# Kernel optimization log

Hardware: AMD Instinct MI355X
Metric: run time of the kernel (lower is better)

Reference implementation:

```python
import jax, jax.numpy as jnp
import numpy as np

B, S, E, D, H, L, V = 8, 128, 512, 1024, 16, 4, 32000
DH = D // H
FF = 4 * D
SCALE = 1.0 / (DH ** 0.5)
NEG = -1e30


def _layer_norm(x, g, b, eps=1e-5):
    m = jnp.mean(x, axis=-1, keepdims=True)
    v = jnp.mean((x - m) ** 2, axis=-1, keepdims=True)
    return (x - m) / jnp.sqrt(v + eps) * g + b


def _rel_shift(x):
    # x: [q, k, b, n] -> TransformerXL relative shift
    q, k, b, n = x.shape
    xp = jnp.concatenate([jnp.zeros((q, 1, b, n), x.dtype), x], axis=1)
    xp = xp.reshape(k + 1, q, b, n)
    return xp[1:].reshape(q, k, b, n)


def setup_inputs():
    key = jax.random.key(0)
    ks = jax.random.split(key, 40)
    g = lambda i, shape, s=0.02: jax.random.normal(ks[i], shape, jnp.float32) * s
    inp = {
        'input_ids': jax.random.randint(ks[0], (B, E), 0, V),
        'encoder_rep': jax.random.normal(ks[1], (B, E, D), jnp.float32),
        'input_mask': jnp.ones((B, E), jnp.float32),
        'decode_input': jax.random.randint(ks[2], (B, S), 0, V),
        'decode_target': jax.random.randint(ks[3], (B, S), 0, V),
        'word_emb': g(4, (V, D)),
        'qkv_w': g(5, (L, 3 * D, D)), 'r_w': g(6, (L, D, D)), 'o_w': g(7, (L, D, D)),
        'kv_w': g(8, (L, 2 * D, D)), 'q_w': g(9, (L, D, D)), 'io_w': g(10, (L, D, D)),
        'rr_bias': g(11, (L, H, DH)), 'rw_bias': g(12, (L, H, DH)),
        'ln1_g': jnp.ones((L, D)), 'ln1_b': jnp.zeros((L, D)),
        'ln2_g': jnp.ones((L, D)), 'ln2_b': jnp.zeros((L, D)),
        'ffn_w1': g(13, (L, FF, D)), 'ffn_b1': jnp.zeros((L, FF)),
        'ffn_w2': g(14, (L, D, FF)), 'ffn_b2': jnp.zeros((L, D)),
        'ln3_g': jnp.ones((L, D)), 'ln3_b': jnp.zeros((L, D)),
        'out_w': g(15, (D, D)), 'out_b': jnp.zeros((D,)),
        'copy_w': g(16, (D, D)), 'copy_b': jnp.zeros((D,)),
        'mode_w': g(17, (1, D)), 'mode_b': jnp.zeros((1,)),
    }
    return inp


def _forward(input_ids, encoder_rep, input_mask, decode_input, decode_target,
             word_emb, qkv_w, r_w, o_w, kv_w, q_w, io_w, rr_bias, rw_bias,
             ln1_g, ln1_b, ln2_g, ln2_b, ffn_w1, ffn_b1, ffn_w2, ffn_b2,
             ln3_g, ln3_b, out_w, out_b, copy_w, copy_b, mode_w, mode_b):
    # relative position embedding r: [S, D]
    pos_seq = jnp.arange(S - 1, -1, -1.0, dtype=jnp.float32)
    inv_freq = 1.0 / (10000.0 ** (jnp.arange(0.0, D, 2.0) / D))
    sin_inp = pos_seq[:, None] * inv_freq[None, :]
    r = jnp.concatenate([jnp.sin(sin_inp), jnp.cos(sin_inp)], axis=-1)

    causal = jnp.tril(jnp.ones((S, S), jnp.bool_))[:, :, None, None]  # [i,j,1,1]
    enc_mask_t = input_mask.T  # [E, B]

    core = word_emb[decode_input].transpose(1, 0, 2)  # [S, B, D]
    enc_t = encoder_rep.transpose(1, 0, 2)            # [E, B, D]

    for l in range(L):
        w = core
        heads = w @ qkv_w[l].T  # [S,B,3D]
        q, k, v = jnp.split(heads, 3, axis=-1)
        q = q.reshape(S, B, H, DH); k = k.reshape(S, B, H, DH); v = v.reshape(S, B, H, DH)
        r_k = (r @ r_w[l].T).reshape(S, H, DH)
        AC = jnp.einsum('ibnd,jbnd->ijbn', q + rw_bias[l], k)
        BD = _rel_shift(jnp.einsum('ibnd,jnd->ijbn', q + rr_bias[l], r_k))
        score = (AC + BD) * SCALE
        score = jnp.where(causal, score, NEG)
        prob = jax.nn.softmax(score, axis=1)
        vec = jnp.einsum('ijbn,jbnd->ibnd', prob, v).reshape(S, B, D)
        x = _layer_norm(w + vec @ o_w[l].T, ln1_g[l], ln1_b[l])

        # cross attention
        kv = enc_t @ kv_w[l].T
        k2, v2 = jnp.split(kv, 2, axis=-1)
        k2 = k2.reshape(E, B, H, DH); v2 = v2.reshape(E, B, H, DH)
        q2 = (x @ q_w[l].T).reshape(S, B, H, DH)
        score2 = jnp.einsum('qbnd,kbnd->qkbn', q2, k2) * SCALE
        score2 = score2 + (1.0 - enc_mask_t)[None, :, :, None] * NEG
        prob2 = jax.nn.softmax(score2, axis=1)
        vec2 = jnp.einsum('ijbn,jbnd->ibnd', prob2, v2).reshape(S, B, D)
        y = _layer_norm(x + vec2 @ io_w[l].T, ln2_g[l], ln2_b[l])

        # FFN (exact GELU as torch nn.GELU default)
        h = jax.nn.gelu(y @ ffn_w1[l].T + ffn_b1[l], approximate=False)
        h = h @ ffn_w2[l].T + ffn_b2[l]
        core = _layer_norm(y + h, ln3_g[l], ln3_b[l])

    core_out = core.transpose(1, 0, 2)  # [B, S, D]
    output = core_out @ out_w.T + out_b
    vocab_logits = output @ word_emb.T  # [B,S,V]
    vocab_prob = jax.nn.softmax(vocab_logits, axis=-1)

    copy_h = core_out @ copy_w.T + copy_b
    input_logits = jnp.einsum('bid,bjd->bij', copy_h, encoder_rep)
    input_logits = input_logits + (1.0 - input_mask[:, None, :]) * NEG
    input_prob = jax.nn.softmax(input_logits, axis=-1)  # [B,S,E]

    mode_sig = jax.nn.sigmoid(core_out @ mode_w.T + mode_b)  # [B,S,1]
    vocab_prob = vocab_prob * mode_sig

    idx = jnp.broadcast_to(input_ids[:, None, :], (B, S, E))
    b_i = jnp.arange(B)[:, None, None]
    s_i = jnp.arange(S)[None, :, None]
    vocab_prob = vocab_prob.at[b_i, s_i, idx].add((1.0 - mode_sig) * input_prob)

    flat = vocab_prob.reshape(-1, V)
    tgt = decode_target.reshape(-1)
    predict = jnp.take_along_axis(flat, tgt[:, None], axis=1)[:, 0]
    valid = (tgt != 0).astype(jnp.float32)
    loss = jnp.sum(-jnp.log(predict + 1e-6) * valid) / jnp.sum(valid)
    return jnp.repeat(loss[None], B)


def reference(input_ids, encoder_rep, input_mask, decode_input, decode_target,
              word_emb, qkv_w, r_w, o_w, kv_w, q_w, io_w, rr_bias, rw_bias,
              ln1_g, ln1_b, ln2_g, ln2_b, ffn_w1, ffn_b1, ffn_w2, ffn_b2,
              ln3_g, ln3_b, out_w, out_b, copy_w, copy_b, mode_w, mode_b):
    return _forward(input_ids, encoder_rep, input_mask, decode_input, decode_target,
                    word_emb, qkv_w, r_w, o_w, kv_w, q_w, io_w, rr_bias, rw_bias,
                    ln1_g, ln1_b, ln2_g, ln2_b, ffn_w1, ffn_b1, ffn_w2, ffn_b2,
                    ln3_g, ln3_b, out_w, out_b, copy_w, copy_b, mode_w, mode_b)
```

## Files before the change

kernel.cpp:

```cpp
#include <hip/hip_runtime.h>
#include <math.h>

#define B_ 8
#define S_ 128
#define E_ 512
#define D_ 1024
#define H_ 16
#define L_ 4
#define V_ 32000
#define DH_ 64
#define FF_ 4096
#define M_ 1024
#define ME_ 4096
#define NT_ 125
#define SCALE_F 0.125f
#define NEGV (-1e30f)

typedef __attribute__((ext_vector_type(8))) short short8;
typedef __attribute__((ext_vector_type(4))) float f32x4;

__device__ __forceinline__ float bf2f(ushort u) {
  union { unsigned int u32; float f; } v; v.u32 = ((unsigned int)u) << 16; return v.f;
}
__device__ __forceinline__ ushort f2bf(float x) {
  union { float f; unsigned int u; } v; v.f = x;
  unsigned int r = v.u + 0x7fff + ((v.u >> 16) & 1);
  return (ushort)(r >> 16);
}
__device__ __forceinline__ void gl_lds16(const ushort* g, ushort* l) {
  __builtin_amdgcn_global_load_lds((const __attribute__((address_space(1))) void*)g,
                                   (__attribute__((address_space(3))) void*)l, 16, 0, 0);
}

__device__ __forceinline__ float warp_reduce_sum(float v) {
#pragma unroll
  for (int o = 32; o > 0; o >>= 1) v += __shfl_down(v, o);
  return v;
}
__device__ __forceinline__ float warp_reduce_max(float v) {
#pragma unroll
  for (int o = 32; o > 0; o >>= 1) v = fmaxf(v, __shfl_down(v, o));
  return v;
}
__device__ __forceinline__ float block_reduce_sum(float v, float* sred) {
  v = warp_reduce_sum(v);
  __syncthreads();
  if ((threadIdx.x & 63) == 0) sred[threadIdx.x >> 6] = v;
  __syncthreads();
  float s = 0.0f;
  int nw = blockDim.x >> 6;
  for (int w = 0; w < nw; ++w) s += sred[w];
  return s;
}
__device__ __forceinline__ float block_reduce_max(float v, float* sred) {
  v = warp_reduce_max(v);
  __syncthreads();
  if ((threadIdx.x & 63) == 0) sred[threadIdx.x >> 6] = v;
  __syncthreads();
  float s = -3.4e38f;
  int nw = blockDim.x >> 6;
  for (int w = 0; w < nw; ++w) s = fmaxf(s, sred[w]);
  return s;
}

__global__ __launch_bounds__(256) void castf_kernel(const float* __restrict__ in,
                                                    ushort* __restrict__ out, int n4) {
  int t = blockIdx.x * 256 + threadIdx.x;
  if (t >= n4) return;
  float4 v = ((const float4*)in)[t];
  ushort4 o;
  o.x = f2bf(v.x); o.y = f2bf(v.y); o.z = f2bf(v.z); o.w = f2bf(v.w);
  ((ushort4*)out)[t] = o;
}

__global__ __launch_bounds__(256) void castlayer_kernel(
    const float* __restrict__ sqkv, const float* __restrict__ so,
    const float* __restrict__ sq, const float* __restrict__ sio,
    const float* __restrict__ sf1, const float* __restrict__ sf2,
    ushort* __restrict__ dqkv, ushort* __restrict__ dov,
    ushort* __restrict__ dq, ushort* __restrict__ dio,
    ushort* __restrict__ df1, ushort* __restrict__ df2) {
  int t = blockIdx.x * 256 + threadIdx.x;
  const float* src; ushort* dst; int idx;
  if (t < 786432)       { src = sqkv; dst = dqkv; idx = t; }
  else if (t < 1048576) { src = so;  dst = dov; idx = t - 786432; }
  else if (t < 1310720) { src = sq;  dst = dq;  idx = t - 1048576; }
  else if (t < 1572864) { src = sio; dst = dio; idx = t - 1310720; }
  else if (t < 2621440) { src = sf1; dst = df1; idx = t - 1572864; }
  else if (t < 3670016) { src = sf2; dst = df2; idx = t - 2621440; }
  else return;
  float4 v = ((const float4*)src)[idx];
  ushort4 o4;
  o4.x = f2bf(v.x); o4.y = f2bf(v.y); o4.z = f2bf(v.z); o4.w = f2bf(v.w);
  ((ushort4*)dst)[idx] = o4;
}

__global__ __launch_bounds__(256) void enc_both_kernel(const float* __restrict__ enc,
                                                       ushort* __restrict__ enc_bf,
                                                       ushort* __restrict__ encT) {
  int t = blockIdx.x * 256 + threadIdx.x;
  if (t >= ME_ * D_) return;
  ushort bv = f2bf(enc[t]);
  enc_bf[t] = bv;
  int d = t & (D_ - 1);
  int be = t >> 10;
  int b = be >> 9, e = be & (E_ - 1);
  encT[((size_t)(e * B_ + b) << 10) + d] = bv;
}

__global__ __launch_bounds__(256) void pos_emb_kernel(ushort* __restrict__ r) {
  int t = blockIdx.x * 256 + threadIdx.x;
  if (t >= S_ * D_) return;
  int i = t / D_, j = t % D_;
  float pos = (float)(S_ - 1 - i);
  int jj = (j < D_ / 2) ? j : (j - D_ / 2);
  float invf = powf(10000.0f, -(float)(2 * jj) / (float)D_);
  float a = pos * invf;
  r[t] = f2bf((j < D_ / 2) ? sinf(a) : cosf(a));
}

__global__ __launch_bounds__(256) void embed_kernel(const int* __restrict__ ids,
                                                    const float* __restrict__ emb,
                                                    float* __restrict__ core,
                                                    ushort* __restrict__ core_bf) {
  int t = blockIdx.x * 256 + threadIdx.x;
  if (t >= M_ * D_) return;
  int d = t & (D_ - 1);
  int row = t >> 10;
  int s = row >> 3, b = row & 7;
  float v = emb[(size_t)ids[b * S_ + s] * D_ + d];
  core[t] = v;
  core_bf[t] = f2bf(v);
}

template <int EPI>
__global__ __launch_bounds__(256) void gemm_w_kernel(
    const ushort* __restrict__ A, const ushort* __restrict__ Bm,
    const float* __restrict__ bias, void* __restrict__ Cv,
    int M, int N, int K, int ksplit,
    long long Arow, long long Abatch, long long Brow, long long Bbatch,
    long long Crow, long long Cbatch, long long Csplit) {
  __shared__ ushort lA[128 * 32];
  __shared__ ushort lB[128 * 32];
  int tid = threadIdx.x;
  int bz = blockIdx.z;
  int batch = bz / ksplit, split = bz % ksplit;
  int kLen = K / ksplit, kStart = split * kLen;
  const ushort* Ab = A + (size_t)batch * Abatch;
  const ushort* Bb = Bm + (size_t)batch * Bbatch;
  int bm = blockIdx.y * 128, bn = blockIdx.x * 128;
  int lane = tid & 63, wave = tid >> 6;
  int wrow = (wave >> 1) * 64, wcol = (wave & 1) * 64;
  int quad = lane >> 4, l16 = lane & 15;
  f32x4 acc[4][4];
#pragma unroll
  for (int i = 0; i < 4; ++i)
#pragma unroll
    for (int j = 0; j < 4; ++j) { acc[i][j][0] = 0.f; acc[i][j][1] = 0.f; acc[i][j][2] = 0.f; acc[i][j][3] = 0.f; }
  int r0 = tid >> 2, c0 = (tid & 3) * 8;
  int r1 = (tid + 256) >> 2;
  for (int k0 = kStart; k0 < kStart + kLen; k0 += 32) {
    __syncthreads();
    gl_lds16(Ab + (size_t)(bm + r0) * Arow + k0 + c0, &lA[(size_t)tid * 8]);
    gl_lds16(Ab + (size_t)(bm + r1) * Arow + k0 + c0, &lA[(size_t)(256 + tid) * 8]);
    gl_lds16(Bb + (size_t)(bn + r0) * Brow + k0 + c0, &lB[(size_t)tid * 8]);
    gl_lds16(Bb + (size_t)(bn + r1) * Brow + k0 + c0, &lB[(size_t)(256 + tid) * 8]);
    __syncthreads();
    short8 af[4], bfr[4];
#pragma unroll
    for (int mi = 0; mi < 4; ++mi)
      af[mi] = *(const short8*)&lA[(size_t)(wrow + mi * 16 + l16) * 32 + quad * 8];
#pragma unroll
    for (int ni = 0; ni < 4; ++ni)
      bfr[ni] = *(const short8*)&lB[(size_t)(wcol + ni * 16 + l16) * 32 + quad * 8];
#pragma unroll
    for (int mi = 0; mi < 4; ++mi)
#pragma unroll
      for (int ni = 0; ni < 4; ++ni)
        acc[mi][ni] = __builtin_amdgcn_mfma_f32_16x16x32_bf16(af[mi], bfr[ni], acc[mi][ni], 0, 0, 0);
  }
#pragma unroll
  for (int mi = 0; mi < 4; ++mi) {
    int row0 = bm + wrow + mi * 16 + quad * 4;
#pragma unroll
    for (int ni = 0; ni < 4; ++ni) {
      int col = bn + wcol + ni * 16 + l16;
      float bv = 0.f;
      if (EPI >= 3) bv = bias[col];
#pragma unroll
      for (int r = 0; r < 4; ++r) {
        float v = acc[mi][ni][r] + bv;
        if (EPI == 4) v = 0.5f * v * (1.0f + erff(v * 0.70710678118654752f));
        size_t ci = (size_t)split * Csplit + (size_t)batch * Cbatch + (size_t)(row0 + r) * Crow + col;
        if (EPI == 0) ((float*)Cv)[ci] = v;
        else ((ushort*)Cv)[ci] = f2bf(v);
      }
    }
  }
}

template <int EPI>
__global__ __launch_bounds__(512, 2) void gemm256_kernel(
    const ushort* __restrict__ A, const ushort* __restrict__ Bm, void* __restrict__ Cv,
    float* __restrict__ tmax, float* __restrict__ tsum,
    long long Arow, long long Abatch, long long Brow, long long Bbatch,
    long long Crow, long long Cbatch) {
  __shared__ ushort sT[2][2][2][128 * 32];
  __shared__ float smax[256][4];
  __shared__ float ssum[256][4];
  const int NK = 32;
  int tid = threadIdx.x;
  int bm, bn, bnT = 0, batch = 0;
  if constexpr (EPI == 5) {
    int orig = blockIdx.x;
    int xcd = orig & 7;
    int base = (xcd < 4) ? xcd * 63 : 4 * 63 + (xcd - 4) * 62;
    int wg = base + (orig >> 3);
    bm = (wg & 3) * 256;
    bnT = wg >> 2;
    bn = bnT * 256;
  } else {
    bn = blockIdx.x * 256;
    bm = blockIdx.y * 256;
    batch = blockIdx.z;
  }
  const ushort* Ab = A + (size_t)batch * Abatch;
  const ushort* Bb = Bm + (size_t)batch * Bbatch;
  int lane = tid & 63, wave = tid >> 6;
  int wr = wave >> 2;
  int wc = wave & 3;
  int bhalf = wc >> 1;
  int brow0 = (wc & 1) * 64;
  int quad = lane >> 4, l16 = lane & 15;
  int sr = tid >> 2;
  int sslot = (((tid & 3) ^ ((sr >> 1) & 3)) * 8);
  int rsw = (quad ^ ((l16 >> 1) & 3)) * 8;

  f32x4 acc[8][4];
#pragma unroll
  for (int i = 0; i < 8; ++i)
#pragma unroll
    for (int j = 0; j < 4; ++j) { acc[i][j][0]=0.f; acc[i][j][1]=0.f; acc[i][j][2]=0.f; acc[i][j][3]=0.f; }

#define STAGE_TILE(s_)                                                                 \
  do {                                                                                 \
    int s__ = (s_); int b__ = s__ & 1;                                                 \
    gl_lds16(Ab + (size_t)(bm + sr) * Arow + s__ * 32 + sslot,                         \
             &sT[b__][0][0][tid * 8]);                                                 \
    gl_lds16(Ab + (size_t)(bm + 128 + sr) * Arow + s__ * 32 + sslot,                   \
             &sT[b__][0][1][tid * 8]);                                                 \
    gl_lds16(Bb + (size_t)(bn + sr) * Brow + s__ * 32 + sslot,                         \
             &sT[b__][1][0][tid * 8]);                                                 \
    gl_lds16(Bb + (size_t)(bn + 128 + sr) * Brow + s__ * 32 + sslot,                   \
             &sT[b__][1][1][tid * 8]);                                                 \
  } while (0)

  STAGE_TILE(0);
  STAGE_TILE(1);
  asm volatile("s_waitcnt vmcnt(4)" ::: "memory");
  __builtin_amdgcn_s_barrier();
  __builtin_amdgcn_sched_barrier(0);

  for (int t = 0; t < NK; ++t) {
    int bt = t & 1;
    short8 af[8], bfv[4];
#pragma unroll
    for (int i = 0; i < 8; ++i)
      af[i] = *(const short8*)&sT[bt][0][wr][(i * 16 + l16) * 32 + rsw];
#pragma unroll
    for (int i = 0; i < 4; ++i)
      bfv[i] = *(const short8*)&sT[bt][1][bhalf][(brow0 + i * 16 + l16) * 32 + rsw];
    __builtin_amdgcn_s_setprio(1);
#pragma unroll
    for (int mi = 0; mi < 8; ++mi)
#pragma unroll
      for (int ni = 0; ni < 4; ++ni)
        acc[mi][ni] = __builtin_amdgcn_mfma_f32_16x16x32_bf16(af[mi], bfv[ni], acc[mi][ni], 0, 0, 0);
    __builtin_amdgcn_s_setprio(0);
    __builtin_amdgcn_s_barrier();
    __builtin_amdgcn_sched_barrier(0);
    if (t + 2 < NK) {
      STAGE_TILE(t + 2);
      asm volatile("s_waitcnt vmcnt(4)" ::: "memory");
    } else {
      asm volatile("s_waitcnt vmcnt(0)" ::: "memory");
    }
    __builtin_amdgcn_s_barrier();
    __builtin_amdgcn_sched_barrier(0);
  }
#undef STAGE_TILE

  if constexpr (EPI == 5) {
#pragma unroll
    for (int mi = 0; mi < 8; ++mi)
#pragma unroll
      for (int r = 0; r < 4; ++r) {
        int rr = wr * 128 + mi * 16 + quad * 4 + r;
        float lm = -3.4e38f;
#pragma unroll
        for (int ni = 0; ni < 4; ++ni) lm = fmaxf(lm, acc[mi][ni][r]);
#pragma unroll
        for (int o = 1; o < 16; o <<= 1) lm = fmaxf(lm, __shfl_xor(lm, o));
        if (l16 == 0) smax[rr][wc] = lm;
      }
    __syncthreads();
#pragma unroll
    for (int mi = 0; mi < 8; ++mi)
#pragma unroll
      for (int r = 0; r < 4; ++r) {
        int rr = wr * 128 + mi * 16 + quad * 4 + r;
        float m = fmaxf(fmaxf(smax[rr][0], smax[rr][1]), fmaxf(smax[rr][2], smax[rr][3]));
        float ls = 0.f;
#pragma unroll
        for (int ni = 0; ni < 4; ++ni) ls += __expf(acc[mi][ni][r] - m);
#pragma unroll
        for (int o = 1; o < 16; o <<= 1) ls += __shfl_xor(ls, o);
        if (l16 == 0) ssum[rr][wc] = ls;
      }
    __syncthreads();
    if (tid < 256) {
      float m = fmaxf(fmaxf(smax[tid][0], smax[tid][1]), fmaxf(smax[tid][2], smax[tid][3]));
      float s = ssum[tid][0] + ssum[tid][1] + ssum[tid][2] + ssum[tid][3];
      tmax[(size_t)(bm + tid) * NT_ + bnT] = m;
      tsum[(size_t)(bm + tid) * NT_ + bnT] = s;
    }
  } else {
    ushort* C = (ushort*)Cv + (size_t)batch * Cbatch;
#pragma unroll
    for (int mi = 0; mi < 8; ++mi) {
      int row0 = bm + wr * 128 + mi * 16 + quad * 4;
#pragma unroll
      for (int ni = 0; ni < 4; ++ni) {
        int col = bn + wc * 64 + ni * 16 + l16;
#pragma unroll
        for (int r = 0; r < 4; ++r)
          C[(size_t)(row0 + r) * Crow + col] = f2bf(acc[mi][ni][r]);
      }
    }
  }
}

__global__ __launch_bounds__(256) void vocab_combine_kernel(const float* __restrict__ tmax,
                                                            const float* __restrict__ tsum,
                                                            const ushort* __restrict__ headout,
                                                            const ushort* __restrict__ emb,
                                                            const int* __restrict__ tgt,
                                                            float* __restrict__ rmax,
                                                            float* __restrict__ rsum,
                                                            float* __restrict__ tl) {
  __shared__ float sred[4];
  int m = blockIdx.x;
  float mx = -3.4e38f;
  for (int t = threadIdx.x; t < NT_; t += 256) mx = fmaxf(mx, tmax[(size_t)m * NT_ + t]);
  mx = block_reduce_max(mx, sred);
  float s = 0.f;
  for (int t = threadIdx.x; t < NT_; t += 256)
    s += tsum[(size_t)m * NT_ + t] * expf(tmax[(size_t)m * NT_ + t] - mx);
  s = block_reduce_sum(s, sred);
  int si = m >> 3, b = m & 7;
  int t = tgt[b * S_ + si];
  const ushort* a = headout + (size_t)m * 2048;
  const ushort* w = emb + (size_t)t * D_;
  float acc = 0.f;
  for (int i = threadIdx.x; i < D_; i += 256) acc += bf2f(a[i]) * bf2f(w[i]);
  acc = block_reduce_sum(acc, sred);
  if (threadIdx.x == 0) { rmax[m] = mx; rsum[m] = s; tl[m] = acc; }
}

__global__ __launch_bounds__(256) void attn1_fused_kernel(const ushort* __restrict__ heads,
                                                          const ushort* __restrict__ rkproj,
                                                          const float* __restrict__ rw,
                                                          const float* __restrict__ rr,
                                                          ushort* __restrict__ attnA) {
  __shared__ float score[128][129];
  __shared__ ushort pP[128][136];
  __shared__ ushort vT[64][136];
  int bz = blockIdx.x;
  int b = bz >> 4, n = bz & 15;
  int tid = threadIdx.x, lane = tid & 63, wave = tid >> 6;
  int quad = lane >> 4, l16 = lane & 15;
  int wrow = wave * 32;

  {
    int j = tid >> 1, dbase = (tid & 1) * 32;
    const ushort* src = heads + (size_t)(j * 8 + b) * 3072 + 2048 + n * 64 + dbase;
#pragma unroll
    for (int c8 = 0; c8 < 4; ++c8) {
      short8 v8 = *(const short8*)(src + c8 * 8);
#pragma unroll
      for (int cc = 0; cc < 8; ++cc) vT[dbase + c8 * 8 + cc][j] = (ushort)v8[cc];
    }
  }

  short8 qrw[2][2], qrr[2][2];
#pragma unroll
  for (int mi = 0; mi < 2; ++mi) {
    int i = wrow + mi * 16 + l16;
    const ushort* qp = heads + (size_t)(i * 8 + b) * 3072 + n * 64;
#pragma unroll
    for (int kc = 0; kc < 2; ++kc) {
      int k0 = kc * 32 + quad * 8;
      short8 qv = *(const short8*)(qp + k0);
      short8 w, rv;
#pragma unroll
      for (int t = 0; t < 8; ++t) {
        float q = bf2f((ushort)qv[t]);
        w[t] = (short)f2bf(q + rw[n * 64 + k0 + t]);
        rv[t] = (short)f2bf(q + rr[n * 64 + k0 + t]);
      }
      qrw[mi][kc] = w; qrr[mi][kc] = rv;
    }
  }

  {
    f32x4 acc[2][8];
#pragma unroll
    for (int i = 0; i < 2; ++i)
#pragma unroll
      for (int j = 0; j < 8; ++j) { acc[i][j][0]=0.f; acc[i][j][1]=0.f; acc[i][j][2]=0.f; acc[i][j][3]=0.f; }
#pragma unroll
    for (int kc = 0; kc < 2; ++kc) {
      int k0 = kc * 32 + quad * 8;
      short8 kf[8];
#pragma unroll
      for (int ni = 0; ni < 8; ++ni) {
        int j = ni * 16 + l16;
        kf[ni] = *(const short8*)(heads + (size_t)(j * 8 + b) * 3072 + 1024 + n * 64 + k0);
      }
#pragma unroll
      for (int mi = 0; mi < 2; ++mi)
#pragma unroll
        for (int ni = 0; ni < 8; ++ni)
          acc[mi][ni] = __builtin_amdgcn_mfma_f32_16x16x32_bf16(qrw[mi][kc], kf[ni], acc[mi][ni], 0, 0, 0);
    }
#pragma unroll
    for (int mi = 0; mi < 2; ++mi)
#pragma unroll
      for (int ni = 0; ni < 8; ++ni)
#pragma unroll
        for (int r = 0; r < 4; ++r)
          score[wrow + mi * 16 + quad * 4 + r][ni * 16 + l16] = acc[mi][ni][r];
  }
  {
    f32x4 acc[2][8];
#pragma unroll
    for (int i = 0; i < 2; ++i)
#pragma unroll
      for (int j = 0; j < 8; ++j) { acc[i][j][0]=0.f; acc[i][j][1]=0.f; acc[i][j][2]=0.f; acc[i][j][3]=0.f; }
#pragma unroll
    for (int kc = 0; kc < 2; ++kc) {
      int k0 = kc * 32 + quad * 8;
      short8 rkf[8];
#pragma unroll
      for (int ni = 0; ni < 8; ++ni) {
        int jp = ni * 16 + l16;
        rkf[ni] = *(const short8*)(rkproj + (size_t)jp * 1024 + n * 64 + k0);
      }
#pragma unroll
      for (int mi = 0; mi < 2; ++mi)
#pragma unroll
        for (int ni = 0; ni < 8; ++ni)
          acc[mi][ni] = __builtin_amdgcn_mfma_f32_16x16x32_bf16(qrr[mi][kc], rkf[ni], acc[mi][ni], 0, 0, 0);
    }
#pragma unroll
    for (int mi = 0; mi < 2; ++mi)
#pragma unroll
      for (int r = 0; r < 4; ++r) {
        int i = wrow + mi * 16 + quad * 4 + r;
#pragma unroll
        for (int ni = 0; ni < 8; ++ni) {
          int jp = ni * 16 + l16;
          if (jp >= 127 - i) score[i][jp - 127 + i] += acc[mi][ni][r];
        }
      }
  }
  {
    int row = tid >> 1, halfc = (tid & 1) * 64;
    float mx = -3.4e38f;
    for (int c = halfc; c < halfc + 64; ++c) {
      float v = (c <= row) ? score[row][c] * SCALE_F : -3.4e38f;
      mx = fmaxf(mx, v);
    }
    mx = fmaxf(mx, __shfl_xor(mx, 1));
    float s = 0.f;
    for (int c = halfc; c < halfc + 64; ++c) {
      float e = (c <= row) ? __expf(score[row][c] * SCALE_F - mx) : 0.f;
      score[row][c] = e;
      s += e;
    }
    s += __shfl_xor(s, 1);
    float inv = 1.0f / s;
    for (int c = halfc; c < halfc + 64; ++c) pP[row][c] = f2bf(score[row][c] * inv);
  }
  __syncthreads();
  {
    f32x4 acc[2][4];
#pragma unroll
    for (int i = 0; i < 2; ++i)
#pragma unroll
      for (int j = 0; j < 4; ++j) { acc[i][j][0]=0.f; acc[i][j][1]=0.f; acc[i][j][2]=0.f; acc[i][j][3]=0.f; }
#pragma unroll
    for (int kc = 0; kc < 4; ++kc) {
      int k0 = kc * 32 + quad * 8;
      short8 pf[2], vf[4];
#pragma unroll
      for (int mi = 0; mi < 2; ++mi)
        pf[mi] = *(const short8*)&pP[wrow + mi * 16 + l16][k0];
#pragma unroll
      for (int ni = 0; ni < 4; ++ni)
        vf[ni] = *(const short8*)&vT[ni * 16 + l16][k0];
#pragma unroll
      for (int mi = 0; mi < 2; ++mi)
#pragma unroll
        for (int ni = 0; ni < 4; ++ni)
          acc[mi][ni] = __builtin_amdgcn_mfma_f32_16x16x32_bf16(pf[mi], vf[ni], acc[mi][ni], 0, 0, 0);
    }
#pragma unroll
    for (int mi = 0; mi < 2; ++mi)
#pragma unroll
      for (int r = 0; r < 4; ++r) {
        int i = wrow + mi * 16 + quad * 4 + r;
#pragma unroll
        for (int ni = 0; ni < 4; ++ni)
          attnA[(size_t)(i * 8 + b) * 1024 + n * 64 + ni * 16 + l16] = f2bf(acc[mi][ni][r]);
      }
  }
}

__global__ __launch_bounds__(256) void attn2_fused_kernel(const float* __restrict__ q0,
                                                          const float* __restrict__ q1,
                                                          const ushort* __restrict__ kvproj,
                                                          const float* __restrict__ mask,
                                                          ushort* __restrict__ attnA) {
  __shared__ ushort vT[64][136];
  __shared__ ushort pP[128][136];
  __shared__ float mtile[128];
  int bz = blockIdx.x;
  int b = bz >> 4, n = bz & 15;
  int tid = threadIdx.x, lane = tid & 63, wave = tid >> 6;
  int quad = lane >> 4, l16 = lane & 15;
  int wrow = wave * 32;
  short8 qf[2][2];
#pragma unroll
  for (int mi = 0; mi < 2; ++mi) {
    int i = wrow + mi * 16 + l16;
    size_t base = (size_t)(i * 8 + b) * 1024 + n * 64;
#pragma unroll
    for (int kc = 0; kc < 2; ++kc) {
      int k0 = kc * 32 + quad * 8;
      short8 v;
#pragma unroll
      for (int t = 0; t < 8; ++t) v[t] = (short)f2bf(q0[base + k0 + t] + q1[base + k0 + t]);
      qf[mi][kc] = v;
    }
  }
  float m_run[2][4], l_run[2][4];
#pragma unroll
  for (int mi = 0; mi < 2; ++mi)
#pragma unroll
    for (int r = 0; r < 4; ++r) { m_run[mi][r] = -3.0e38f; l_run[mi][r] = 0.f; }
  f32x4 accO[2][4];
#pragma unroll
  for (int i = 0; i < 2; ++i)
#pragma unroll
    for (int j = 0; j < 4; ++j) { accO[i][j][0]=0.f; accO[i][j][1]=0.f; accO[i][j][2]=0.f; accO[i][j][3]=0.f; }

  for (int et = 0; et < 4; ++et) {
    __syncthreads();
    {
      int j = tid >> 1, dbase = (tid & 1) * 32;
      int e = et * 128 + j;
      const ushort* src = kvproj + (size_t)(e * 8 + b) * 2048 + 1024 + n * 64 + dbase;
#pragma unroll
      for (int c8 = 0; c8 < 4; ++c8) {
        short8 v8 = *(const short8*)(src + c8 * 8);
#pragma unroll
        for (int cc = 0; cc < 8; ++cc) vT[dbase + c8 * 8 + cc][j] = (ushort)v8[cc];
      }
      if (tid < 128) mtile[tid] = (1.0f - mask[b * E_ + et * 128 + tid]) * NEGV;
    }
    f32x4 accS[2][8];
#pragma unroll
    for (int i = 0; i < 2; ++i)
#pragma unroll
      for (int j = 0; j < 8; ++j) { accS[i][j][0]=0.f; accS[i][j][1]=0.f; accS[i][j][2]=0.f; accS[i][j][3]=0.f; }
#pragma unroll
    for (int kc = 0; kc < 2; ++kc) {
      int k0 = kc * 32 + quad * 8;
      short8 kf[8];
#pragma unroll
      for (int ni = 0; ni < 8; ++ni) {
        int e = et * 128 + ni * 16 + l16;
        kf[ni] = *(const short8*)(kvproj + (size_t)(e * 8 + b) * 2048 + n * 64 + k0);
      }
#pragma unroll
      for (int mi = 0; mi < 2; ++mi)
#pragma unroll
        for (int ni = 0; ni < 8; ++ni)
          accS[mi][ni] = __builtin_amdgcn_mfma_f32_16x16x32_bf16(qf[mi][kc], kf[ni], accS[mi][ni], 0, 0, 0);
    }
    __syncthreads();
#pragma unroll
    for (int mi = 0; mi < 2; ++mi)
#pragma unroll
      for (int r = 0; r < 4; ++r) {
        float v[8];
        float vmax = -3.4e38f;
#pragma unroll
        for (int ni = 0; ni < 8; ++ni) {
          v[ni] = accS[mi][ni][r] * SCALE_F + mtile[ni * 16 + l16];
          vmax = fmaxf(vmax, v[ni]);
        }
#pragma unroll
        for (int o = 1; o < 16; o <<= 1) vmax = fmaxf(vmax, __shfl_xor(vmax, o));
        float mnew = fmaxf(m_run[mi][r], vmax);
        float alpha = __expf(m_run[mi][r] - mnew);
        float ls = 0.f;
        int row = wrow + mi * 16 + quad * 4 + r;
#pragma unroll
        for (int ni = 0; ni < 8; ++ni) {
          float p = __expf(v[ni] - mnew);
          ls += p;
          pP[row][ni * 16 + l16] = f2bf(p);
        }
#pragma unroll
        for (int o = 1; o < 16; o <<= 1) ls += __shfl_xor(ls, o);
        l_run[mi][r] = l_run[mi][r] * alpha + ls;
        m_run[mi][r] = mnew;
#pragma unroll
        for (int ni = 0; ni < 4; ++ni) accO[mi][ni][r] *= alpha;
      }
#pragma unroll
    for (int kc = 0; kc < 4; ++kc) {
      int k0 = kc * 32 + quad * 8;
      short8 pf[2], vf[4];
#pragma unroll
      for (int mi = 0; mi < 2; ++mi)
        pf[mi] = *(const short8*)&pP[wrow + mi * 16 + l16][k0];
#pragma unroll
      for (int ni = 0; ni < 4; ++ni)
        vf[ni] = *(const short8*)&vT[ni * 16 + l16][k0];
#pragma unroll
      for (int mi = 0; mi < 2; ++mi)
#pragma unroll
        for (int ni = 0; ni < 4; ++ni)
          accO[mi][ni] = __builtin_amdgcn_mfma_f32_16x16x32_bf16(pf[mi], vf[ni], accO[mi][ni], 0, 0, 0);
    }
  }
#pragma unroll
  for (int mi = 0; mi < 2; ++mi)
#pragma unroll
    for (int r = 0; r < 4; ++r) {
      int i = wrow + mi * 16 + quad * 4 + r;
      float inv = 1.0f / l_run[mi][r];
#pragma unroll
      for (int ni = 0; ni < 4; ++ni)
        attnA[(size_t)(i * 8 + b) * 1024 + n * 64 + ni * 16 + l16] = f2bf(accO[mi][ni][r] * inv);
    }
}

__global__ __launch_bounds__(256) void addln_kernel(const float* __restrict__ a,
                                                    const float* __restrict__ c,
                                                    int nsplit, long long cstride,
                                                    const float* __restrict__ bias,
                                                    const float* __restrict__ g,
                                                    const float* __restrict__ bb,
                                                    float* __restrict__ out,
                                                    ushort* __restrict__ out_bf,
                                                    const float* __restrict__ mw,
                                                    const float* __restrict__ mb,
                                                    float* __restrict__ msig) {
  __shared__ float sred[4];
  int row = blockIdx.x;
  const float* pa = a + (size_t)row * D_;
  float vals[4];
  float s = 0.f;
#pragma unroll
  for (int it = 0; it < 4; ++it) {
    int idx = threadIdx.x + it * 256;
    float v = pa[idx];
    for (int sp = 0; sp < nsplit; ++sp) v += c[(size_t)sp * cstride + (size_t)row * D_ + idx];
    if (bias) v += bias[idx];
    vals[it] = v;
    s += v;
  }
  s = block_reduce_sum(s, sred);
  float mean = s * (1.0f / D_);
  float ss = 0.f;
#pragma unroll
  for (int it = 0; it < 4; ++it) {
    float dd = vals[it] - mean;
    ss += dd * dd;
  }
  ss = block_reduce_sum(ss, sred);
  float inv = rsqrtf(ss * (1.0f / D_) + 1e-5f);
#pragma unroll
  for (int it = 0; it < 4; ++it) {
    int idx = threadIdx.x + it * 256;
    float r = (vals[it] - mean) * inv * g[idx] + bb[idx];
    vals[it] = r;
    out[(size_t)row * D_ + idx] = r;
    out_bf[(size_t)row * D_ + idx] = f2bf(r);
  }
  if (mw) {
    float sm = 0.f;
#pragma unroll
    for (int it = 0; it < 4; ++it) {
      int idx = threadIdx.x + it * 256;
      sm += vals[it] * mw[idx];
    }
    sm = block_reduce_sum(sm, sred);
    if (threadIdx.x == 0) msig[row] = 1.0f / (1.0f + expf(-(sm + mb[0])));
  }
}

__global__ __launch_bounds__(256) void final_kernel(const float* __restrict__ lg,
                                                    const int* __restrict__ ids,
                                                    const float* __restrict__ mask,
                                                    const int* __restrict__ tgt,
                                                    const float* __restrict__ mode_sig,
                                                    const float* __restrict__ tlogit,
                                                    const float* __restrict__ rmax,
                                                    const float* __restrict__ rsum,
                                                    float* __restrict__ loss_acc) {
  __shared__ float sred[4];
  int s = blockIdx.x, b = blockIdx.y;
  int m = s * B_ + b;
  size_t base = (size_t)(b * S_ + s) * E_;
  const long long LGS = (long long)B_ * S_ * E_;
  int tg = tgt[b * S_ + s];
  float lv[2];
  float mx = -3.4e38f;
#pragma unroll
  for (int it = 0; it < 2; ++it) {
    int e = threadIdx.x + it * 256;
    float raw = 0.f;
#pragma unroll
    for (int sp = 0; sp < 4; ++sp) raw += lg[sp * LGS + base + e];
    raw += (1.0f - mask[b * E_ + e]) * NEGV;
    lv[it] = raw;
    mx = fmaxf(mx, raw);
  }
  mx = block_reduce_max(mx, sred);
  float ssum = 0.f, csum = 0.f;
#pragma unroll
  for (int it = 0; it < 2; ++it) {
    int e = threadIdx.x + it * 256;
    float ev = expf(lv[it] - mx);
    ssum += ev;
    if (ids[b * E_ + e] == tg) csum += ev;
  }
  ssum = block_reduce_sum(ssum, sred);
  csum = block_reduce_sum(csum, sred);
  if (threadIdx.x == 0) {
    float copy_p = csum / ssum;
    float pv = expf(tlogit[m] - rmax[m]) / rsum[m];
    float msig = mode_sig[m];
    float predict = pv * msig + (1.0f - msig) * copy_p;
    float valid = (tg != 0) ? 1.0f : 0.0f;
    atomicAdd(&loss_acc[0], -logf(predict + 1e-6f) * valid);
    atomicAdd(&loss_acc[1], valid);
  }
}

__global__ void writeout_kernel(const float* __restrict__ loss_acc, float* __restrict__ out) {
  if (threadIdx.x < B_) out[threadIdx.x] = loss_acc[0] / loss_acc[1];
}

static void gw(hipStream_t st, int epi, const ushort* A, const ushort* B, const float* bias,
               void* C, int M, int N, int K,
               long long Ar, long long Ab, long long Br, long long Bb,
               long long Cr, long long Cb, int nb, int ksplit, long long Csplit) {
  dim3 g(N / 128, M / 128, nb * ksplit);
  switch (epi) {
    case 0: gemm_w_kernel<0><<<g, 256, 0, st>>>(A, B, bias, C, M, N, K, ksplit, Ar, Ab, Br, Bb, Cr, Cb, Csplit); break;
    case 1: gemm_w_kernel<1><<<g, 256, 0, st>>>(A, B, bias, C, M, N, K, ksplit, Ar, Ab, Br, Bb, Cr, Cb, Csplit); break;
    case 3: gemm_w_kernel<3><<<g, 256, 0, st>>>(A, B, bias, C, M, N, K, ksplit, Ar, Ab, Br, Bb, Cr, Cb, Csplit); break;
    case 4: gemm_w_kernel<4><<<g, 256, 0, st>>>(A, B, bias, C, M, N, K, ksplit, Ar, Ab, Br, Bb, Cr, Cb, Csplit); break;
  }
}
static void castTo(hipStream_t st, const float* src, ushort* dst, size_t count) {
  int n4 = (int)(count / 4);
  castf_kernel<<<(n4 + 255) / 256, 256, 0, st>>>(src, dst, n4);
}

extern "C" void kernel_launch(void* const* d_in, const int* in_sizes, int n_in,
                              void* d_out, int out_size, void* d_ws, size_t ws_size,
                              hipStream_t stream) {
  const int* input_ids = (const int*)d_in[0];
  const float* encoder_rep = (const float*)d_in[1];
  const float* input_mask = (const float*)d_in[2];
  const int* decode_input = (const int*)d_in[3];
  const int* decode_target = (const int*)d_in[4];
  const float* word_emb = (const float*)d_in[5];
  const float* qkv_w = (const float*)d_in[6];
  const float* r_w = (const float*)d_in[7];
  const float* o_w = (const float*)d_in[8];
  const float* kv_w = (const float*)d_in[9];
  const float* q_w = (const float*)d_in[10];
  const float* io_w = (const float*)d_in[11];
  const float* rr_bias = (const float*)d_in[12];
  const float* rw_bias = (const float*)d_in[13];
  const float* ln1_g = (const float*)d_in[14];
  const float* ln1_b = (const float*)d_in[15];
  const float* ln2_g = (const float*)d_in[16];
  const float* ln2_b = (const float*)d_in[17];
  const float* ffn_w1 = (const float*)d_in[18];
  const float* ffn_b1 = (const float*)d_in[19];
  const float* ffn_w2 = (const float*)d_in[20];
  const float* ffn_b2 = (const float*)d_in[21];
  const float* ln3_g = (const float*)d_in[22];
  const float* ln3_b = (const float*)d_in[23];
  const float* out_w = (const float*)d_in[24];
  const float* out_b = (const float*)d_in[25];
  const float* copy_w = (const float*)d_in[26];
  const float* copy_b = (const float*)d_in[27];
  const float* mode_w = (const float*)d_in[28];
  const float* mode_b = (const float*)d_in[29];
  float* out = (float*)d_out;

  char* base = (char*)d_ws;
  size_t off = 0;
  auto alloc = [&](size_t bytes) -> void* {
    void* p = base + off;
    off = (off + bytes + 255) & ~(size_t)255;
    return p;
  };

  ushort* wl_qkv = (ushort*)alloc((size_t)3 * D_ * D_ * 2);
  ushort* wl_o = (ushort*)alloc((size_t)D_ * D_ * 2);
  ushort* wl_q = (ushort*)alloc((size_t)D_ * D_ * 2);
  ushort* wl_io = (ushort*)alloc((size_t)D_ * D_ * 2);
  ushort* wl_f1 = (ushort*)alloc((size_t)FF_ * D_ * 2);
  ushort* wl_f2 = (ushort*)alloc((size_t)FF_ * D_ * 2);
  ushort* wl_kv = (ushort*)alloc((size_t)L_ * 2 * D_ * D_ * 2);
  ushort* wl_r = (ushort*)alloc((size_t)L_ * D_ * D_ * 2);
  ushort* kvproj_bf = (ushort*)alloc((size_t)L_ * ME_ * 2 * D_ * 2);
  ushort* rkproj_bf = (ushort*)alloc((size_t)L_ * S_ * D_ * 2);

  ushort* w_emb = (ushort*)alloc((size_t)V_ * D_ * 2);
  ushort* w_oc = (ushort*)alloc((size_t)2048 * D_ * 2);
  float* b_oc = (float*)alloc(2048 * 4);
  ushort* enc_bf = (ushort*)alloc((size_t)ME_ * D_ * 2);
  ushort* encT_bf = (ushort*)alloc((size_t)ME_ * D_ * 2);
  ushort* r_bf = (ushort*)alloc((size_t)S_ * D_ * 2);
  float* f_core = (float*)alloc((size_t)M_ * D_ * 4);
  ushort* core_bf = (ushort*)alloc((size_t)M_ * D_ * 2);
  ushort* heads_bf = (ushort*)alloc((size_t)M_ * 3 * D_ * 2);
  ushort* attnA_bf = (ushort*)alloc((size_t)M_ * D_ * 2);
  float* f_tmp = (float*)alloc((size_t)4 * M_ * D_ * 4);
  float* f_x = (float*)alloc((size_t)M_ * D_ * 4);
  ushort* x_bf = (ushort*)alloc((size_t)M_ * D_ * 2);
  float* f_y = (float*)alloc((size_t)M_ * D_ * 4);
  ushort* y_bf = (ushort*)alloc((size_t)M_ * D_ * 2);
  float* f_q = (float*)alloc((size_t)2 * M_ * D_ * 4);
  ushort* ffnh_bf = (ushort*)alloc((size_t)M_ * FF_ * 2);
  ushort* headout_bf = (ushort*)alloc((size_t)M_ * 2048 * 2);
  float* f_lg = (float*)alloc((size_t)4 * B_ * S_ * E_ * 4);
  float* f_tmax = (float*)alloc((size_t)M_ * NT_ * 4);
  float* f_tsum = (float*)alloc((size_t)M_ * NT_ * 4);
  float* f_rmax = (float*)alloc(M_ * 4);
  float* f_rsum = (float*)alloc(M_ * 4);
  float* f_tlogit = (float*)alloc(M_ * 4);
  float* f_mode = (float*)alloc(M_ * 4);
  float* f_loss = (float*)alloc(64);

  castTo(stream, word_emb, w_emb, (size_t)V_ * D_);
  castTo(stream, out_w, w_oc, (size_t)D_ * D_);
  castTo(stream, copy_w, w_oc + (size_t)D_ * D_, (size_t)D_ * D_);
  hipMemcpyAsync(b_oc, out_b, D_ * 4, hipMemcpyDeviceToDevice, stream);
  hipMemcpyAsync(b_oc + D_, copy_b, D_ * 4, hipMemcpyDeviceToDevice, stream);
  enc_both_kernel<<<(ME_ * D_) / 256, 256, 0, stream>>>(encoder_rep, enc_bf, encT_bf);
  pos_emb_kernel<<<(S_ * D_ + 255) / 256, 256, 0, stream>>>(r_bf);
  embed_kernel<<<(M_ * D_) / 256, 256, 0, stream>>>(decode_input, word_emb, f_core, core_bf);

  castTo(stream, kv_w, wl_kv, (size_t)L_ * 2 * D_ * D_);
  castTo(stream, r_w, wl_r, (size_t)L_ * D_ * D_);
  gemm256_kernel<1><<<dim3(2 * D_ / 256, ME_ / 256, L_), 512, 0, stream>>>(
      encT_bf, wl_kv, kvproj_bf, nullptr, nullptr,
      D_, 0, D_, (long long)2 * D_ * D_, 2 * D_, (long long)ME_ * 2 * D_);
  gw(stream, 1, r_bf, wl_r, nullptr, rkproj_bf, S_, D_, D_,
     D_, 0, D_, (long long)D_ * D_, D_, (long long)S_ * D_, L_, 1, 0);

  for (int l = 0; l < L_; ++l) {
    castlayer_kernel<<<14336, 256, 0, stream>>>(
        qkv_w + (size_t)l * 3 * D_ * D_, o_w + (size_t)l * D_ * D_,
        q_w + (size_t)l * D_ * D_, io_w + (size_t)l * D_ * D_,
        ffn_w1 + (size_t)l * FF_ * D_, ffn_w2 + (size_t)l * FF_ * D_,
        wl_qkv, wl_o, wl_q, wl_io, wl_f1, wl_f2);

    gw(stream, 1, core_bf, wl_qkv, nullptr, heads_bf, M_, 3 * D_, D_, D_, 0, D_, 0, 3 * D_, 0, 1, 1, 0);
    attn1_fused_kernel<<<B_ * H_, 256, 0, stream>>>(heads_bf, rkproj_bf + (size_t)l * S_ * D_,
                                                    rw_bias + (size_t)l * D_,
                                                    rr_bias + (size_t)l * D_, attnA_bf);
    gw(stream, 0, attnA_bf, wl_o, nullptr, f_tmp, M_, D_, D_, D_, 0, D_, 0, D_, 0, 1, 2,
       (long long)M_ * D_);
    addln_kernel<<<M_, 256, 0, stream>>>(f_core, f_tmp, 2, (long long)M_ * D_, nullptr,
                                         ln1_g + (size_t)l * D_, ln1_b + (size_t)l * D_, f_x, x_bf,
                                         nullptr, nullptr, nullptr);

    gw(stream, 0, x_bf, wl_q, nullptr, f_q, M_, D_, D_, D_, 0, D_, 0, D_, 0, 1, 2,
       (long long)M_ * D_);
    attn2_fused_kernel<<<B_ * H_, 256, 0, stream>>>(f_q, f_q + (size_t)M_ * D_,
                                                    kvproj_bf + (size_t)l * ME_ * 2 * D_,
                                                    input_mask, attnA_bf);
    gw(stream, 0, attnA_bf, wl_io, nullptr, f_tmp, M_, D_, D_, D_, 0, D_, 0, D_, 0, 1, 2,
       (long long)M_ * D_);
    addln_kernel<<<M_, 256, 0, stream>>>(f_x, f_tmp, 2, (long long)M_ * D_, nullptr,
                                         ln2_g + (size_t)l * D_, ln2_b + (size_t)l * D_, f_y, y_bf,
                                         nullptr, nullptr, nullptr);

    gw(stream, 4, y_bf, wl_f1, ffn_b1 + (size_t)l * FF_, ffnh_bf, M_, FF_, D_, D_, 0, D_, 0, FF_, 0, 1, 1, 0);
    gw(stream, 0, ffnh_bf, wl_f2, nullptr, f_tmp, M_, D_, FF_, FF_, 0, FF_, 0, D_, 0, 1, 4,
       (long long)M_ * D_);
    bool last = (l == L_ - 1);
    addln_kernel<<<M_, 256, 0, stream>>>(f_y, f_tmp, 4, (long long)M_ * D_,
                                         ffn_b2 + (size_t)l * D_,
                                         ln3_g + (size_t)l * D_, ln3_b + (size_t)l * D_, f_core, core_bf,
                                         last ? mode_w : nullptr, last ? mode_b : nullptr,
                                         last ? f_mode : nullptr);
  }

  gw(stream, 3, core_bf, w_oc, b_oc, headout_bf, M_, 2048, D_, D_, 0, D_, 0, 2048, 0, 1, 1, 0);

  gemm256_kernel<5><<<500, 512, 0, stream>>>(headout_bf, w_emb, nullptr, f_tmax, f_tsum,
                                             2048, 0, D_, 0, 0, 0);
  vocab_combine_kernel<<<M_, 256, 0, stream>>>(f_tmax, f_tsum, headout_bf, w_emb, decode_target,
                                               f_rmax, f_rsum, f_tlogit);

  gw(stream, 0, headout_bf + D_, enc_bf, nullptr, f_lg, S_, E_, D_,
     (long long)B_ * 2048, 2048, D_, (long long)E_ * D_, E_, (long long)S_ * E_, B_, 4,
     (long long)B_ * S_ * E_);

  hipMemsetAsync(f_loss, 0, 2 * sizeof(float), stream);
  final_kernel<<<dim3(S_, B_), 256, 0, stream>>>(f_lg, input_ids, input_mask, decode_target,
                                                 f_mode, f_tlogit, f_rmax, f_rsum, f_loss);
  writeout_kernel<<<1, 64, 0, stream>>>(f_loss, out);
}
```

Measured before the change: 1.583 ms.

## Deepen gemm256 LDS pipeline to four stages and fuse vocab combine into final loss

The 256x256 GEMM now keeps four LDS tile buffers and prefetches three K-steps ahead, aiming to hide more global load latency. The vocab softmax combine and target-logit dot product are folded into the final loss kernel, which removes one launch and its intermediate buffers. The out/copy weight casts and bias copies are merged into a single kernel. Doubling LDS per block risks halving the resident blocks per CU.

```diff
diff --git a/kernel.cpp b/kernel.cpp
--- a/kernel.cpp
+++ b/kernel.cpp
@@ -71,6 +71,28 @@
   ushort4 o;
   o.x = f2bf(v.x); o.y = f2bf(v.y); o.z = f2bf(v.z); o.w = f2bf(v.w);
   ((ushort4*)out)[t] = o;
+}
+
+__global__ __launch_bounds__(256) void castoc_kernel(const float* __restrict__ ow,
+                                                     const float* __restrict__ cw,
+                                                     const float* __restrict__ ob,
+                                                     const float* __restrict__ cb,
+                                                     ushort* __restrict__ w_oc,
+                                                     float* __restrict__ b_oc) {
+  int t = blockIdx.x * 256 + threadIdx.x;
+  if (t < 524288) {
+    const float* src = (t < 262144) ? ow : cw;
+    int idx = (t < 262144) ? t : t - 262144;
+    float4 v = ((const float4*)src)[idx];
+    ushort4 o4;
+    o4.x = f2bf(v.x); o4.y = f2bf(v.y); o4.z = f2bf(v.z); o4.w = f2bf(v.w);
+    ((ushort4*)w_oc)[t] = o4;
+  }
+  if (t < 512) {
+    const float* bsrc = (t < 256) ? ob : cb;
+    int bi = (t < 256) ? t : t - 256;
+    ((float4*)b_oc)[t] = ((const float4*)bsrc)[bi];
+  }
 }
 
 __global__ __launch_bounds__(256) void castlayer_kernel(
@@ -205,7 +227,7 @@
     float* __restrict__ tmax, float* __restrict__ tsum,
     long long Arow, long long Abatch, long long Brow, long long Bbatch,
     long long Crow, long long Cbatch) {
-  __shared__ ushort sT[2][2][2][128 * 32];
+  __shared__ ushort sT[4][2][2][128 * 32];
   __shared__ float smax[256][4];
   __shared__ float ssum[256][4];
   const int NK = 32;
@@ -244,7 +266,7 @@
 
 #define STAGE_TILE(s_)                                                                 \
   do {                                                                                 \
-    int s__ = (s_); int b__ = s__ & 1;                                                 \
+    int s__ = (s_); int b__ = s__ & 3;                                                 \
     gl_lds16(Ab + (size_t)(bm + sr) * Arow + s__ * 32 + sslot,                         \
              &sT[b__][0][0][tid * 8]);                                                 \
     gl_lds16(Ab + (size_t)(bm + 128 + sr) * Arow + s__ * 32 + sslot,                   \
@@ -257,12 +279,13 @@
 
   STAGE_TILE(0);
   STAGE_TILE(1);
-  asm volatile("s_waitcnt vmcnt(4)" ::: "memory");
+  STAGE_TILE(2);
+  asm volatile("s_waitcnt vmcnt(8)" ::: "memory");
   __builtin_amdgcn_s_barrier();
   __builtin_amdgcn_sched_barrier(0);
 
   for (int t = 0; t < NK; ++t) {
-    int bt = t & 1;
+    int bt = t & 3;
     short8 af[8], bfv[4];
 #pragma unroll
     for (int i = 0; i < 8; ++i)
@@ -279,8 +302,10 @@
     __builtin_amdgcn_s_setprio(0);
     __builtin_amdgcn_s_barrier();
     __builtin_amdgcn_sched_barrier(0);
-    if (t + 2 < NK) {
-      STAGE_TILE(t + 2);
+    if (t + 3 < NK) {
+      STAGE_TILE(t + 3);
+      asm volatile("s_waitcnt vmcnt(8)" ::: "memory");
+    } else if (t + 2 < NK) {
       asm volatile("s_waitcnt vmcnt(4)" ::: "memory");
     } else {
       asm volatile("s_waitcnt vmcnt(0)" ::: "memory");
@@ -338,33 +363,6 @@
       }
     }
   }
-}
-
-__global__ __launch_bounds__(256) void vocab_combine_kernel(const float* __restrict__ tmax,
-                                                            const float* __restrict__ tsum,
-                                                            const ushort* __restrict__ headout,
-                                                            const ushort* __restrict__ emb,
-                                                            const int* __restrict__ tgt,
-                                                            float* __restrict__ rmax,
-                                                            float* __restrict__ rsum,
-                                                            float* __restrict__ tl) {
-  __shared__ float sred[4];
-  int m = blockIdx.x;
-  float mx = -3.4e38f;
-  for (int t = threadIdx.x; t < NT_; t += 256) mx = fmaxf(mx, tmax[(size_t)m * NT_ + t]);
-  mx = block_reduce_max(mx, sred);
-  float s = 0.f;
-  for (int t = threadIdx.x; t < NT_; t += 256)
-    s += tsum[(size_t)m * NT_ + t] * expf(tmax[(size_t)m * NT_ + t] - mx);
-  s = block_reduce_sum(s, sred);
-  int si = m >> 3, b = m & 7;
-  int t = tgt[b * S_ + si];
-  const ushort* a = headout + (size_t)m * 2048;
-  const ushort* w = emb + (size_t)t * D_;
-  float acc = 0.f;
-  for (int i = threadIdx.x; i < D_; i += 256) acc += bf2f(a[i]) * bf2f(w[i]);
-  acc = block_reduce_sum(acc, sred);
-  if (threadIdx.x == 0) { rmax[m] = mx; rsum[m] = s; tl[m] = acc; }
 }
 
 __global__ __launch_bounds__(256) void attn1_fused_kernel(const ushort* __restrict__ heads,
@@ -714,21 +712,34 @@
   }
 }
 
-__global__ __launch_bounds__(256) void final_kernel(const float* __restrict__ lg,
-                                                    const int* __restrict__ ids,
-                                                    const float* __restrict__ mask,
-                                                    const int* __restrict__ tgt,
-                                                    const float* __restrict__ mode_sig,
-                                                    const float* __restrict__ tlogit,
-                                                    const float* __restrict__ rmax,
-                                                    const float* __restrict__ rsum,
-                                                    float* __restrict__ loss_acc) {
+__global__ __launch_bounds__(256) void final2_kernel(const float* __restrict__ tmax,
+                                                     const float* __restrict__ tsum,
+                                                     const ushort* __restrict__ headout,
+                                                     const ushort* __restrict__ emb,
+                                                     const float* __restrict__ lg,
+                                                     const int* __restrict__ ids,
+                                                     const float* __restrict__ mask,
+                                                     const int* __restrict__ tgt,
+                                                     const float* __restrict__ mode_sig,
+                                                     float* __restrict__ loss_acc) {
   __shared__ float sred[4];
   int s = blockIdx.x, b = blockIdx.y;
   int m = s * B_ + b;
+  int tg = tgt[b * S_ + s];
+  float vmx = -3.4e38f;
+  for (int t = threadIdx.x; t < NT_; t += 256) vmx = fmaxf(vmx, tmax[(size_t)m * NT_ + t]);
+  vmx = block_reduce_max(vmx, sred);
+  float vsum = 0.f;
+  for (int t = threadIdx.x; t < NT_; t += 256)
+    vsum += tsum[(size_t)m * NT_ + t] * expf(tmax[(size_t)m * NT_ + t] - vmx);
+  vsum = block_reduce_sum(vsum, sred);
+  const ushort* a = headout + (size_t)m * 2048;
+  const ushort* w = emb + (size_t)tg * D_;
+  float tl = 0.f;
+  for (int i = threadIdx.x; i < D_; i += 256) tl += bf2f(a[i]) * bf2f(w[i]);
+  tl = block_reduce_sum(tl, sred);
   size_t base = (size_t)(b * S_ + s) * E_;
   const long long LGS = (long long)B_ * S_ * E_;
-  int tg = tgt[b * S_ + s];
   float lv[2];
   float mx = -3.4e38f;
 #pragma unroll
@@ -754,7 +765,7 @@
   csum = block_reduce_sum(csum, sred);
   if (threadIdx.x == 0) {
     float copy_p = csum / ssum;
-    float pv = expf(tlogit[m] - rmax[m]) / rsum[m];
+    float pv = expf(tl - vmx) / vsum;
     float msig = mode_sig[m];
     float predict = pv * msig + (1.0f - msig) * copy_p;
     float valid = (tg != 0) ? 1.0f : 0.0f;
@@ -859,17 +870,11 @@
   float* f_lg = (float*)alloc((size_t)4 * B_ * S_ * E_ * 4);
   float* f_tmax = (float*)alloc((size_t)M_ * NT_ * 4);
   float* f_tsum = (float*)alloc((size_t)M_ * NT_ * 4);
-  float* f_rmax = (float*)alloc(M_ * 4);
-  float* f_rsum = (float*)alloc(M_ * 4);
-  float* f_tlogit = (float*)alloc(M_ * 4);
   float* f_mode = (float*)alloc(M_ * 4);
   float* f_loss = (float*)alloc(64);
 
   castTo(stream, word_emb, w_emb, (size_t)V_ * D_);
-  castTo(stream, out_w, w_oc, (size_t)D_ * D_);
-  castTo(stream, copy_w, w_oc + (size_t)D_ * D_, (size_t)D_ * D_);
-  hipMemcpyAsync(b_oc, out_b, D_ * 4, hipMemcpyDeviceToDevice, stream);
-  hipMemcpyAsync(b_oc + D_, copy_b, D_ * 4, hipMemcpyDeviceToDevice, stream);
+  castoc_kernel<<<2048, 256, 0, stream>>>(out_w, copy_w, out_b, copy_b, w_oc, b_oc);
   enc_both_kernel<<<(ME_ * D_) / 256, 256, 0, stream>>>(encoder_rep, enc_bf, encT_bf);
   pos_emb_kernel<<<(S_ * D_ + 255) / 256, 256, 0, stream>>>(r_bf);
   embed_kernel<<<(M_ * D_) / 256, 256, 0, stream>>>(decode_input, word_emb, f_core, core_bf);
@@ -925,15 +930,14 @@
 
   gemm256_kernel<5><<<500, 512, 0, stream>>>(headout_bf, w_emb, nullptr, f_tmax, f_tsum,
                                              2048, 0, D_, 0, 0, 0);
-  vocab_combine_kernel<<<M_, 256, 0, stream>>>(f_tmax, f_tsum, headout_bf, w_emb, decode_target,
-                                               f_rmax, f_rsum, f_tlogit);
 
   gw(stream, 0, headout_bf + D_, enc_bf, nullptr, f_lg, S_, E_, D_,
      (long long)B_ * 2048, 2048, D_, (long long)E_ * D_, E_, (long long)S_ * E_, B_, 4,
      (long long)B_ * S_ * E_);
 
   hipMemsetAsync(f_loss, 0, 2 * sizeof(float), stream);
-  final_kernel<<<dim3(S_, B_), 256, 0, stream>>>(f_lg, input_ids, input_mask, decode_target,
-                                                 f_mode, f_tlogit, f_rmax, f_rsum, f_loss);
+  final2_kernel<<<dim3(S_, B_), 256, 0, stream>>>(f_tmax, f_tsum, headout_bf, w_emb, f_lg,
+                                                  input_ids, input_mask, decode_target,
+                                                  f_mode, f_loss);
   writeout_kernel<<<1, 64, 0, stream>>>(f_loss, out);
 }
```

Measured after the change: 1.578 ms. About the same (-0.3%).
